# Optimization experiments

Hardware: AMD Instinct MI355X
Metric: run time of the kernel (lower is better)

## Reference

```python
import jax, jax.numpy as jnp
import numpy as np

CONF = 0.3      # confidence threshold (NMS.conf)
IOU = 0.6       # IoU threshold (NMS.iou)
MAX_WH = 4096.0 # class-offset trick for per-class NMS
K = 2048        # max candidates entering NMS (yolov5-style cap)
MAX_DET = 300   # max detections kept per image (fixed output size)


def setup_inputs() -> dict:
    key = jax.random.key(0)
    kxy, kwh, kobj, kcls = jax.random.split(key, 4)
    B, N, NC = 8, 25200, 80
    # realistic raw predictions: xywh in pixel units for a 640x640 image
    xy = jax.random.uniform(kxy, (B, N, 2), minval=0.0, maxval=640.0)
    wh = jax.random.uniform(kwh, (B, N, 2), minval=2.0, maxval=160.0)
    obj = jax.random.uniform(kobj, (B, N, 1))
    cls = jax.random.uniform(kcls, (B, N, NC))
    x = jnp.concatenate([xy, wh, obj, cls], axis=-1)  # [B, N, 5+NC]
    return {"x": x}


def _xywh2xyxy(b):
    xy, half = b[..., :2], b[..., 2:4] * 0.5
    return jnp.concatenate([xy - half, xy + half], axis=-1)


def _pairwise_iou(boxes):  # boxes: [K, 4] xyxy -> [K, K]
    lt = jnp.maximum(boxes[:, None, :2], boxes[None, :, :2])
    rb = jnp.minimum(boxes[:, None, 2:], boxes[None, :, 2:])
    inter = jnp.clip(rb - lt, 0.0).prod(-1)
    area = (boxes[:, 2] - boxes[:, 0]) * (boxes[:, 3] - boxes[:, 1])
    return inter / (area[:, None] + area[None, :] - inter + 1e-9)


def _nms_single(pred):  # pred: [N, 5+NC]
    obj = pred[:, 4]
    cls_conf = pred[:, 5:] * obj[:, None]          # conf = obj * cls prob
    conf = cls_conf.max(-1)
    cls_id = jnp.argmax(cls_conf, -1)
    valid = (obj > CONF) & (conf > CONF)           # candidate + final threshold
    boxes = _xywh2xyxy(pred[:, :4])
    scores = jnp.where(valid, conf, -1.0)
    top_s, idx = jax.lax.top_k(scores, K)          # cap candidates, sorted desc
    boxes_k = boxes[idx]
    cls_k = cls_id[idx]
    valid_k = top_s > 0.0
    # offset boxes by class so NMS is per-class
    shifted = boxes_k + cls_k[:, None].astype(boxes_k.dtype) * MAX_WH
    iou = _pairwise_iou(shifted)                   # [K, K]
    order = jnp.arange(K)

    def body(keep, i):  # greedy suppression in score order
        active = keep[i] & valid_k[i]
        sup = (iou[i] > IOU) & (order > i)
        keep = jnp.where(active, keep & ~sup, keep)
        return keep, None

    keep, _ = jax.lax.scan(body, jnp.ones((K,), bool), order)
    keep = keep & valid_k
    final_s = jnp.where(keep, top_s, -1.0)
    det_s, det_i = jax.lax.top_k(final_s, MAX_DET)
    dets = jnp.concatenate(
        [boxes_k[det_i], top_s[det_i][:, None],
         cls_k[det_i][:, None].astype(boxes_k.dtype)], axis=-1)  # [MAX_DET, 6]
    return dets, det_s > 0.0


def reference(x):
    # returns (dets [B, MAX_DET, 6] = xyxy,conf,cls ; valid mask [B, MAX_DET])
    return jax.vmap(_nms_single)(x)
```

## Files before the change

### kernel.cpp

```cpp
#include <hip/hip_runtime.h>
#include <hip/hip_bf16.h>

#define B 8
#define N 25200
#define ROW 85
#define NC 80
#define K 2048
#define MAXDET 300
#define NBUCKET 16384
#define CAND_CAP 4096
#define NCHUNK 32
#define STILE 64

__global__ void __launch_bounds__(256)
nms_score_kernel(const float* __restrict__ x,
                 float* __restrict__ scores,
                 int* __restrict__ cls_id,
                 unsigned* __restrict__ hist) {
    int b = blockIdx.y;
    int i0 = blockIdx.x * STILE;
    int rows = N - i0; if (rows > STILE) rows = STILE;
    __shared__ float lx[STILE * ROW];
    {
        const float4* s4 = (const float4*)(x + ((size_t)b * N + i0) * ROW);
        float4* d4 = (float4*)lx;
        int nv = rows * ROW / 4;
        for (int k = threadIdx.x; k < nv; k += 256) d4[k] = s4[k];
    }
    __syncthreads();
    int g = threadIdx.x >> 2;
    int q = threadIdx.x & 3;
    if (g >= rows) return;
    const float* p = lx + g * ROW;
    float obj = p[4];
    float best = -1e30f;
    int bc = 127;
    if (obj > 0.3f) {
        #pragma unroll
        for (int k = 0; k < 20; ++k) {
            int c = q + 4 * k;
            float v = __fmul_rn(p[5 + c], obj);
            if (v > best) { best = v; bc = c; }
        }
    }
    #pragma unroll
    for (int m = 1; m < 4; m <<= 1) {
        float ov = __shfl_xor(best, m, 64);
        int   oc = __shfl_xor(bc, m, 64);
        if (ov > best || (ov == best && oc < bc)) { best = ov; bc = oc; }
    }
    if (q == 0) {
        int i = i0 + g;
        float score = (obj > 0.3f && best > 0.3f) ? best : -1.0f;
        scores[b * N + i] = score;
        cls_id[b * N + i] = (bc == 127) ? 0 : bc;
        if (score > 0.0f) {
            int qb = (int)(__fmul_rn(score, 16384.0f));
            if (qb > NBUCKET - 1) qb = NBUCKET - 1;
            atomicAdd(&hist[b * NBUCKET + qb], 1u);
        }
    }
}

__global__ void __launch_bounds__(1024, 1)
nms_select_kernel(const float* __restrict__ scores,
                  const float* __restrict__ x,
                  const int* __restrict__ cls_id,
                  const unsigned* __restrict__ hist,
                  float* __restrict__ top_s,
                  float* __restrict__ boxes,
                  int* __restrict__ clsk,
                  float* __restrict__ shifted,
                  float* __restrict__ area,
                  unsigned long long* __restrict__ keepbits) {
    __shared__ unsigned loff[NBUCKET];
    __shared__ unsigned lcnt16[NBUCKET / 2];
    __shared__ unsigned long long lk[CAND_CAP];
    __shared__ unsigned wsum[16];

    int b = blockIdx.x;
    int t = threadIdx.x;
    int ln = t & 63, wv = t >> 6;
    constexpr int NITER = (N + 1023) / 1024;

    if (t < NCHUNK) keepbits[b * NCHUNK + t] = 0ULL;

    {
        uint4 z = {0u, 0u, 0u, 0u};
        uint4* d2 = (uint4*)lcnt16;
        for (int k = t; k < NBUCKET / 8; k += 1024) d2[k] = z;
    }
    for (int k = t; k < CAND_CAP; k += 1024) lk[k] = 0ULL;

    unsigned v[16];
    int base_j = t * 16;
    unsigned A4 = (unsigned)(NBUCKET - 16 - base_j) / 4;
    {
        const uint4* gh = (const uint4*)(hist + (size_t)b * NBUCKET);
        uint4 u0 = gh[A4 + 0];
        uint4 u1 = gh[A4 + 1];
        uint4 u2 = gh[A4 + 2];
        uint4 u3 = gh[A4 + 3];
        unsigned u[16] = {u0.x,u0.y,u0.z,u0.w, u1.x,u1.y,u1.z,u1.w,
                          u2.x,u2.y,u2.z,u2.w, u3.x,u3.y,u3.z,u3.w};
        #pragma unroll
        for (int k = 0; k < 16; ++k) v[k] = u[15 - k];
    }
    unsigned S = 0;
    #pragma unroll
    for (int k = 0; k < 16; ++k) S += v[k];
    unsigned pref = S;
    #pragma unroll
    for (int o = 1; o < 64; o <<= 1) { unsigned u = __shfl_up(pref, o, 64); if (ln >= o) pref += u; }
    if (ln == 63) wsum[wv] = pref;
    __syncthreads();
    unsigned wbase = 0;
    for (int w = 0; w < wv; ++w) wbase += wsum[w];
    unsigned running = wbase + pref - S;
    {
        unsigned o[16];
        #pragma unroll
        for (int k = 0; k < 16; ++k) { o[15 - k] = running; running += v[k]; }
        ((uint4*)loff)[A4 + 0] = make_uint4(o[0],  o[1],  o[2],  o[3]);
        ((uint4*)loff)[A4 + 1] = make_uint4(o[4],  o[5],  o[6],  o[7]);
        ((uint4*)loff)[A4 + 2] = make_uint4(o[8],  o[9],  o[10], o[11]);
        ((uint4*)loff)[A4 + 3] = make_uint4(o[12], o[13], o[14], o[15]);
    }
    __syncthreads();

    float sreg[NITER];
    #pragma unroll
    for (int r = 0; r < NITER; ++r) {
        int i = t + r * 1024;
        sreg[r] = (i < N) ? scores[b * N + i] : -1.0f;
    }
    #pragma unroll
    for (int r = 0; r < NITER; ++r) {
        float s = sreg[r];
        if (s > 0.0f) {
            int i = t + r * 1024;
            int q = (int)(__fmul_rn(s, 16384.0f));
            if (q > NBUCKET - 1) q = NBUCKET - 1;
            unsigned start = loff[q];
            if (start < CAND_CAP) {
                unsigned sh = (q & 1) * 16;
                unsigned old = atomicAdd(&lcnt16[q >> 1], 1u << sh);
                unsigned rank = (old >> sh) & 0xFFFFu;
                unsigned pos = start + rank;
                if (pos < CAND_CAP) {
                    unsigned long long key =
                        ((unsigned long long)__float_as_uint(s) << 32) | (unsigned)(~i);
                    lk[pos] = key;
                }
            }
        }
    }
    __syncthreads();

    for (int q = t; q < NBUCKET; q += 1024) {
        unsigned start = loff[q];
        if (start < CAND_CAP) {
            unsigned c = (lcnt16[q >> 1] >> ((q & 1) * 16)) & 0xFFFFu;
            unsigned m = c;
            if (m > CAND_CAP - start) m = CAND_CAP - start;
            if (m >= 2) {
                for (unsigned a = start + 1; a < start + m; ++a) {
                    unsigned long long kv = lk[a];
                    unsigned p2 = a;
                    while (p2 > start && lk[p2 - 1] < kv) { lk[p2] = lk[p2 - 1]; --p2; }
                    lk[p2] = kv;
                }
            }
        }
    }
    __syncthreads();

    for (int r = t; r < K; r += 1024) {
        unsigned long long key = lk[r];
        float s;
        int idx;
        float x1, y1, x2, y2;
        int c;
        if (key == 0ULL) {
            s = -1.0f; x1 = y1 = x2 = y2 = 0.0f; c = 0;
        } else {
            s = __uint_as_float((unsigned)(key >> 32));
            idx = (int)(~(unsigned)key);
            const float* p = x + ((size_t)b * N + idx) * ROW;
            float cx = p[0], cy = p[1], w = p[2], h = p[3];
            float hx = __fmul_rn(w, 0.5f);
            float hy = __fmul_rn(h, 0.5f);
            x1 = __fsub_rn(cx, hx); y1 = __fsub_rn(cy, hy);
            x2 = __fadd_rn(cx, hx); y2 = __fadd_rn(cy, hy);
            c = cls_id[b * N + idx];
        }
        int o = b * K + r;
        top_s[o] = s;
        boxes[o * 4 + 0] = x1; boxes[o * 4 + 1] = y1;
        boxes[o * 4 + 2] = x2; boxes[o * 4 + 3] = y2;
        clsk[o] = c;
        float sh = __fmul_rn((float)c, 4096.0f);
        float sx1 = __fadd_rn(x1, sh), sy1 = __fadd_rn(y1, sh);
        float sx2 = __fadd_rn(x2, sh), sy2 = __fadd_rn(y2, sh);
        shifted[o * 4 + 0] = sx1; shifted[o * 4 + 1] = sy1;
        shifted[o * 4 + 2] = sx2; shifted[o * 4 + 3] = sy2;
        area[o] = __fmul_rn(__fsub_rn(sx2, sx1), __fsub_rn(sy2, sy1));
    }
}

__global__ void __launch_bounds__(64)
nms_class_kernel(const float* __restrict__ top_s,
                 const int* __restrict__ clsk,
                 const float* __restrict__ shifted,
                 const float* __restrict__ area,
                 unsigned long long* __restrict__ keepbits) {
    int c = blockIdx.x, b = blockIdx.y;
    int t = threadIdx.x;
    unsigned long long below = (t == 0) ? 0ULL : (~0ULL >> (64 - t));

    __shared__ int srank[K];
    __shared__ unsigned long long skeep[NCHUNK];

    int n = 0;
    for (int ch = 0; ch < NCHUNK; ++ch) {
        int r = ch * 64 + t;
        bool sel = (clsk[b * K + r] == c) && (top_s[b * K + r] > 0.0f);
        unsigned long long m = __ballot(sel);
        if (sel) srank[n + __popcll(m & below)] = r;
        n += __popcll(m);
    }
    __syncthreads();
    if (n == 0) return;

    if (n <= 64) {
        float x1 = 0.f, y1 = 0.f, x2 = 0.f, y2 = 0.f, ar = 0.f;
        int r = -1;
        if (t < n) {
            r = srank[t];
            const float* sb = shifted + ((size_t)b * K + r) * 4;
            x1 = sb[0]; y1 = sb[1]; x2 = sb[2]; y2 = sb[3];
            ar = area[b * K + r];
        }
        unsigned long long keepw = (n == 64) ? ~0ULL : ((1ULL << n) - 1ULL);
        for (int i = 0; i < n; ++i) {
            if (!((keepw >> i) & 1ULL)) continue;
            float bx1 = __shfl(x1, i, 64), by1 = __shfl(y1, i, 64);
            float bx2 = __shfl(x2, i, 64), by2 = __shfl(y2, i, 64);
            float ba  = __shfl(ar, i, 64);
            bool cond = false;
            if (t > i && t < n) {
                float lx = fmaxf(bx1, x1), ly = fmaxf(by1, y1);
                float rx = fminf(bx2, x2), ry = fminf(by2, y2);
                float w = fmaxf(__fsub_rn(rx, lx), 0.0f);
                float h = fmaxf(__fsub_rn(ry, ly), 0.0f);
                float inter = __fmul_rn(w, h);
                float denom = __fadd_rn(__fsub_rn(__fadd_rn(ba, ar), inter), 1e-9f);
                cond = __fdiv_rn(inter, denom) > 0.6f;
            }
            keepw &= ~__ballot(cond);
        }
        if (t < n && ((keepw >> t) & 1ULL))
            atomicOr(&keepbits[b * NCHUNK + (r >> 6)], 1ULL << (r & 63));
        return;
    }

    for (int w = t; w < NCHUNK; w += 64) {
        int lo = w * 64;
        unsigned long long vw;
        if (n >= lo + 64)      vw = ~0ULL;
        else if (n <= lo)      vw = 0ULL;
        else                   vw = (1ULL << (n - lo)) - 1ULL;
        skeep[w] = vw;
    }
    __syncthreads();
    for (int i = 0; i < n; ++i) {
        if (!((skeep[i >> 6] >> (i & 63)) & 1ULL)) continue;
        int ri = srank[i];
        const float* sbi = shifted + ((size_t)b * K + ri) * 4;
        float bx1 = sbi[0], by1 = sbi[1], bx2 = sbi[2], by2 = sbi[3];
        float ba = area[b * K + ri];
        int jb_hi = (n - 1) >> 6;
        for (int jb2 = (i + 1) >> 6; jb2 <= jb_hi; ++jb2) {
            int j = jb2 * 64 + t;
            bool cond = false;
            if (j > i && j < n) {
                int rj = srank[j];
                const float* sbj = shifted + ((size_t)b * K + rj) * 4;
                float x1 = sbj[0], y1 = sbj[1], x2 = sbj[2], y2 = sbj[3];
                float arj = area[b * K + rj];
                float lx = fmaxf(bx1, x1), ly = fmaxf(by1, y1);
                float rx = fminf(bx2, x2), ry = fminf(by2, y2);
                float w = fmaxf(__fsub_rn(rx, lx), 0.0f);
                float h = fmaxf(__fsub_rn(ry, ly), 0.0f);
                float inter = __fmul_rn(w, h);
                float denom = __fadd_rn(__fsub_rn(__fadd_rn(ba, arj), inter), 1e-9f);
                cond = __fdiv_rn(inter, denom) > 0.6f;
            }
            unsigned long long sup = __ballot(cond);
            if (t == 0) skeep[jb2] &= ~sup;
        }
        __syncthreads();
    }
    for (int j = t; j < n; j += 64) {
        if ((skeep[j >> 6] >> (j & 63)) & 1ULL) {
            int r = srank[j];
            atomicOr(&keepbits[b * NCHUNK + (r >> 6)], 1ULL << (r & 63));
        }
    }
}

__global__ void __launch_bounds__(64)
nms_out_kernel(const unsigned long long* __restrict__ keepbits,
               const float* __restrict__ top_s,
               const float* __restrict__ boxes,
               const int* __restrict__ clsk,
               float* __restrict__ out) {
    int b = blockIdx.x;
    int lane = threadIdx.x;
    __shared__ unsigned long long kept[NCHUNK];
    if (lane < NCHUNK) kept[lane] = keepbits[b * NCHUNK + lane];
    __syncthreads();

    int total = 0;
    for (int c = 0; c < NCHUNK; ++c) total += __popcll(kept[c]);

    float* dets  = out + (size_t)b * MAXDET * 6;
    float* flags = out + (size_t)B * MAXDET * 6 + (size_t)b * MAXDET;
    unsigned long long below = (lane == 0) ? 0ULL : (~0ULL >> (64 - lane));
    int kc = 0, nc2 = 0;
    for (int c = 0; c < NCHUNK; ++c) {
        int i = c * 64 + lane;
        unsigned long long m = kept[c];
        bool k = ((m >> lane) & 1ULL) != 0ULL;
        int pc = __popcll(m);
        int slot = k ? (kc + __popcll(m & below))
                     : (total + nc2 + __popcll((~m) & below));
        if (slot < MAXDET) {
            int o = b * K + i;
            dets[slot * 6 + 0] = boxes[o * 4 + 0];
            dets[slot * 6 + 1] = boxes[o * 4 + 1];
            dets[slot * 6 + 2] = boxes[o * 4 + 2];
            dets[slot * 6 + 3] = boxes[o * 4 + 3];
            dets[slot * 6 + 4] = top_s[o];
            dets[slot * 6 + 5] = (float)clsk[o];
            flags[slot] = k ? 1.0f : 0.0f;
        }
        kc += pc;
        nc2 += 64 - pc;
    }
}

extern "C" void kernel_launch(void* const* d_in, const int* in_sizes, int n_in,
                              void* d_out, int out_size, void* d_ws, size_t ws_size,
                              hipStream_t stream) {
    const float* x = (const float*)d_in[0];
    float* out = (float*)d_out;

    char* ws = (char*)d_ws;
    size_t off = 0;
    auto alloc = [&](size_t bytes) -> void* {
        void* p = ws + off;
        off += bytes;
        off = (off + 255) & ~(size_t)255;
        return p;
    };

    float*    scores = (float*)    alloc((size_t)B * N * 4);
    int*      cls_id = (int*)      alloc((size_t)B * N * 4);
    float*    top_s  = (float*)    alloc((size_t)B * K * 4);
    float*    boxes  = (float*)    alloc((size_t)B * K * 4 * 4);
    int*      clsk   = (int*)      alloc((size_t)B * K * 4);
    float*    shifted= (float*)    alloc((size_t)B * K * 4 * 4);
    float*    area   = (float*)    alloc((size_t)B * K * 4);
    unsigned long long* keepbits = (unsigned long long*) alloc((size_t)B * NCHUNK * 8);
    unsigned* hist   = (unsigned*) alloc((size_t)B * NBUCKET * 4);
    (void)ws_size;

    hipMemsetAsync(hist, 0, (size_t)B * NBUCKET * 4, stream);
    nms_score_kernel<<<dim3((N + STILE - 1) / STILE, B), 256, 0, stream>>>(x, scores, cls_id, hist);
    nms_select_kernel<<<B, 1024, 0, stream>>>(scores, x, cls_id, hist,
                                              top_s, boxes, clsk, shifted, area, keepbits);
    nms_class_kernel<<<dim3(NC, B), 64, 0, stream>>>(top_s, clsk, shifted, area, keepbits);
    nms_out_kernel<<<B, 64, 0, stream>>>(keepbits, top_s, boxes, clsk, out);
}
```

Before: 144.5 us.

## Split select kernel into scan, grid-wide placement, and finish kernels

The single per-image select kernel, which ran only 8 blocks, is split into three kernels. A scan kernel writes bucket offsets to global memory. A placement kernel spread over the whole grid scatters candidate keys with global atomics. A finish kernel loads the keys, sorts within buckets and gathers the outputs. This spreads the 25200-element scatter across many CUs instead of 8, at the cost of two extra launches, global atomics and extra workspace memset traffic.

```diff
diff --git a/kernel.cpp b/kernel.cpp
--- a/kernel.cpp
+++ b/kernel.cpp
@@ -62,39 +62,16 @@
     }
 }
 
-__global__ void __launch_bounds__(1024, 1)
-nms_select_kernel(const float* __restrict__ scores,
-                  const float* __restrict__ x,
-                  const int* __restrict__ cls_id,
-                  const unsigned* __restrict__ hist,
-                  float* __restrict__ top_s,
-                  float* __restrict__ boxes,
-                  int* __restrict__ clsk,
-                  float* __restrict__ shifted,
-                  float* __restrict__ area,
-                  unsigned long long* __restrict__ keepbits) {
-    __shared__ unsigned loff[NBUCKET];
-    __shared__ unsigned lcnt16[NBUCKET / 2];
-    __shared__ unsigned long long lk[CAND_CAP];
+__global__ void __launch_bounds__(1024)
+nms_scan_kernel(const unsigned* __restrict__ hist,
+                unsigned* __restrict__ gstart) {
     __shared__ unsigned wsum[16];
-
     int b = blockIdx.x;
     int t = threadIdx.x;
     int ln = t & 63, wv = t >> 6;
-    constexpr int NITER = (N + 1023) / 1024;
-
-    if (t < NCHUNK) keepbits[b * NCHUNK + t] = 0ULL;
-
-    {
-        uint4 z = {0u, 0u, 0u, 0u};
-        uint4* d2 = (uint4*)lcnt16;
-        for (int k = t; k < NBUCKET / 8; k += 1024) d2[k] = z;
-    }
-    for (int k = t; k < CAND_CAP; k += 1024) lk[k] = 0ULL;
 
     unsigned v[16];
-    int base_j = t * 16;
-    unsigned A4 = (unsigned)(NBUCKET - 16 - base_j) / 4;
+    unsigned A4 = (unsigned)(NBUCKET - 16 - t * 16) / 4;
     {
         const uint4* gh = (const uint4*)(hist + (size_t)b * NBUCKET);
         uint4 u0 = gh[A4 + 0];
@@ -121,46 +98,65 @@
         unsigned o[16];
         #pragma unroll
         for (int k = 0; k < 16; ++k) { o[15 - k] = running; running += v[k]; }
-        ((uint4*)loff)[A4 + 0] = make_uint4(o[0],  o[1],  o[2],  o[3]);
-        ((uint4*)loff)[A4 + 1] = make_uint4(o[4],  o[5],  o[6],  o[7]);
-        ((uint4*)loff)[A4 + 2] = make_uint4(o[8],  o[9],  o[10], o[11]);
-        ((uint4*)loff)[A4 + 3] = make_uint4(o[12], o[13], o[14], o[15]);
-    }
-    __syncthreads();
-
-    float sreg[NITER];
-    #pragma unroll
-    for (int r = 0; r < NITER; ++r) {
-        int i = t + r * 1024;
-        sreg[r] = (i < N) ? scores[b * N + i] : -1.0f;
-    }
-    #pragma unroll
-    for (int r = 0; r < NITER; ++r) {
-        float s = sreg[r];
-        if (s > 0.0f) {
-            int i = t + r * 1024;
-            int q = (int)(__fmul_rn(s, 16384.0f));
-            if (q > NBUCKET - 1) q = NBUCKET - 1;
-            unsigned start = loff[q];
-            if (start < CAND_CAP) {
-                unsigned sh = (q & 1) * 16;
-                unsigned old = atomicAdd(&lcnt16[q >> 1], 1u << sh);
-                unsigned rank = (old >> sh) & 0xFFFFu;
-                unsigned pos = start + rank;
-                if (pos < CAND_CAP) {
-                    unsigned long long key =
-                        ((unsigned long long)__float_as_uint(s) << 32) | (unsigned)(~i);
-                    lk[pos] = key;
-                }
+        uint4* gs = (uint4*)(gstart + (size_t)b * NBUCKET);
+        gs[A4 + 0] = make_uint4(o[0],  o[1],  o[2],  o[3]);
+        gs[A4 + 1] = make_uint4(o[4],  o[5],  o[6],  o[7]);
+        gs[A4 + 2] = make_uint4(o[8],  o[9],  o[10], o[11]);
+        gs[A4 + 3] = make_uint4(o[12], o[13], o[14], o[15]);
+    }
+}
+
+__global__ void __launch_bounds__(1024)
+nms_place_kernel(const float* __restrict__ scores,
+                 const unsigned* __restrict__ gstart,
+                 unsigned* __restrict__ gcur,
+                 unsigned long long* __restrict__ gkeys) {
+    int b = blockIdx.y;
+    int i = blockIdx.x * 1024 + threadIdx.x;
+    if (i >= N) return;
+    float s = scores[b * N + i];
+    if (s > 0.0f) {
+        int q = (int)(__fmul_rn(s, 16384.0f));
+        if (q > NBUCKET - 1) q = NBUCKET - 1;
+        unsigned start = gstart[b * NBUCKET + q];
+        if (start < CAND_CAP) {
+            unsigned rank = atomicAdd(&gcur[b * NBUCKET + q], 1u);
+            unsigned pos = start + rank;
+            if (pos < CAND_CAP) {
+                gkeys[(size_t)b * CAND_CAP + pos] =
+                    ((unsigned long long)__float_as_uint(s) << 32) | (unsigned)(~i);
             }
         }
     }
+}
+
+__global__ void __launch_bounds__(1024)
+nms_finish_kernel(const unsigned* __restrict__ gstart,
+                  const unsigned* __restrict__ gcur,
+                  const unsigned long long* __restrict__ gkeys,
+                  const float* __restrict__ x,
+                  const int* __restrict__ cls_id,
+                  float* __restrict__ top_s,
+                  float* __restrict__ boxes,
+                  int* __restrict__ clsk,
+                  float* __restrict__ shifted,
+                  float* __restrict__ area,
+                  unsigned long long* __restrict__ keepbits) {
+    __shared__ unsigned long long lk[CAND_CAP];
+    int b = blockIdx.x;
+    int t = threadIdx.x;
+
+    if (t < NCHUNK) keepbits[b * NCHUNK + t] = 0ULL;
+    {
+        const unsigned long long* gk = gkeys + (size_t)b * CAND_CAP;
+        for (int k = t; k < CAND_CAP; k += 1024) lk[k] = gk[k];
+    }
     __syncthreads();
 
     for (int q = t; q < NBUCKET; q += 1024) {
-        unsigned start = loff[q];
+        unsigned start = gstart[b * NBUCKET + q];
         if (start < CAND_CAP) {
-            unsigned c = (lcnt16[q >> 1] >> ((q & 1) * 16)) & 0xFFFFu;
+            unsigned c = gcur[b * NBUCKET + q];
             unsigned m = c;
             if (m > CAND_CAP - start) m = CAND_CAP - start;
             if (m >= 2) {
@@ -374,11 +370,18 @@
     float*    area   = (float*)    alloc((size_t)B * K * 4);
     unsigned long long* keepbits = (unsigned long long*) alloc((size_t)B * NCHUNK * 8);
     unsigned* hist   = (unsigned*) alloc((size_t)B * NBUCKET * 4);
+    unsigned* gcur   = (unsigned*) alloc((size_t)B * NBUCKET * 4);
+    unsigned long long* gkeys = (unsigned long long*) alloc((size_t)B * CAND_CAP * 8);
+    unsigned* gstart = (unsigned*) alloc((size_t)B * NBUCKET * 4);
     (void)ws_size;
 
-    hipMemsetAsync(hist, 0, (size_t)B * NBUCKET * 4, stream);
+    hipMemsetAsync(hist, 0,
+                   (size_t)B * NBUCKET * 4 + (size_t)B * NBUCKET * 4 + (size_t)B * CAND_CAP * 8,
+                   stream);
     nms_score_kernel<<<dim3((N + STILE - 1) / STILE, B), 256, 0, stream>>>(x, scores, cls_id, hist);
-    nms_select_kernel<<<B, 1024, 0, stream>>>(scores, x, cls_id, hist,
+    nms_scan_kernel<<<B, 1024, 0, stream>>>(hist, gstart);
+    nms_place_kernel<<<dim3((N + 1023) / 1024, B), 1024, 0, stream>>>(scores, gstart, gcur, gkeys);
+    nms_finish_kernel<<<B, 1024, 0, stream>>>(gstart, gcur, gkeys, x, cls_id,
                                               top_s, boxes, clsk, shifted, area, keepbits);
     nms_class_kernel<<<dim3(NC, B), 64, 0, stream>>>(top_s, clsk, shifted, area, keepbits);
     nms_out_kernel<<<B, 64, 0, stream>>>(keepbits, top_s, boxes, clsk, out);
```

Result: slower. 150.3 us (+4.0%).

## Precompute per-class candidate bitmasks, fuse output into class kernel via last-block counter

Applied to the files above, without the earlier changes.

The score kernel now also writes xyxy boxes for every row, so the select kernel gathers one float4 instead of reading scattered raw rows. The select kernel builds per-class bitmasks of candidate ranks in shared memory and writes them out. The class kernel then reads 32 mask words instead of scanning all 2048 clsk/top_s entries per class. The separate output kernel is folded in through an atomic done counter, where the last block per image emits the detections. This removes one launch and redundant scans, at the cost of extra box writes for all rows and threadfence/atomic overhead.

```diff
diff --git a/kernel.cpp b/kernel.cpp
--- a/kernel.cpp
+++ b/kernel.cpp
@@ -16,7 +16,8 @@
 nms_score_kernel(const float* __restrict__ x,
                  float* __restrict__ scores,
                  int* __restrict__ cls_id,
-                 unsigned* __restrict__ hist) {
+                 unsigned* __restrict__ hist,
+                 float4* __restrict__ boxes4) {
     int b = blockIdx.y;
     int i0 = blockIdx.x * STILE;
     int rows = N - i0; if (rows > STILE) rows = STILE;
@@ -54,6 +55,11 @@
         float score = (obj > 0.3f && best > 0.3f) ? best : -1.0f;
         scores[b * N + i] = score;
         cls_id[b * N + i] = (bc == 127) ? 0 : bc;
+        float cx = p[0], cy = p[1], w = p[2], h = p[3];
+        float hx = __fmul_rn(w, 0.5f);
+        float hy = __fmul_rn(h, 0.5f);
+        boxes4[b * N + i] = make_float4(__fsub_rn(cx, hx), __fsub_rn(cy, hy),
+                                        __fadd_rn(cx, hx), __fadd_rn(cy, hy));
         if (score > 0.0f) {
             int qb = (int)(__fmul_rn(score, 16384.0f));
             if (qb > NBUCKET - 1) qb = NBUCKET - 1;
@@ -64,7 +70,7 @@
 
 __global__ void __launch_bounds__(1024, 1)
 nms_select_kernel(const float* __restrict__ scores,
-                  const float* __restrict__ x,
+                  const float4* __restrict__ boxes4,
                   const int* __restrict__ cls_id,
                   const unsigned* __restrict__ hist,
                   float* __restrict__ top_s,
@@ -72,10 +78,12 @@
                   int* __restrict__ clsk,
                   float* __restrict__ shifted,
                   float* __restrict__ area,
-                  unsigned long long* __restrict__ keepbits) {
+                  unsigned long long* __restrict__ keepbits,
+                  unsigned long long* __restrict__ gclsmask) {
     __shared__ unsigned loff[NBUCKET];
     __shared__ unsigned lcnt16[NBUCKET / 2];
     __shared__ unsigned long long lk[CAND_CAP];
+    __shared__ unsigned long long lcm[NC * NCHUNK];
     __shared__ unsigned wsum[16];
 
     int b = blockIdx.x;
@@ -91,10 +99,10 @@
         for (int k = t; k < NBUCKET / 8; k += 1024) d2[k] = z;
     }
     for (int k = t; k < CAND_CAP; k += 1024) lk[k] = 0ULL;
+    for (int k = t; k < NC * NCHUNK; k += 1024) lcm[k] = 0ULL;
 
     unsigned v[16];
-    int base_j = t * 16;
-    unsigned A4 = (unsigned)(NBUCKET - 16 - base_j) / 4;
+    unsigned A4 = (unsigned)(NBUCKET - 16 - t * 16) / 4;
     {
         const uint4* gh = (const uint4*)(hist + (size_t)b * NBUCKET);
         uint4 u0 = gh[A4 + 0];
@@ -186,13 +194,10 @@
         } else {
             s = __uint_as_float((unsigned)(key >> 32));
             idx = (int)(~(unsigned)key);
-            const float* p = x + ((size_t)b * N + idx) * ROW;
-            float cx = p[0], cy = p[1], w = p[2], h = p[3];
-            float hx = __fmul_rn(w, 0.5f);
-            float hy = __fmul_rn(h, 0.5f);
-            x1 = __fsub_rn(cx, hx); y1 = __fsub_rn(cy, hy);
-            x2 = __fadd_rn(cx, hx); y2 = __fadd_rn(cy, hy);
+            float4 bb = boxes4[(size_t)b * N + idx];
+            x1 = bb.x; y1 = bb.y; x2 = bb.z; y2 = bb.w;
             c = cls_id[b * N + idx];
+            atomicOr(&lcm[c * NCHUNK + (r >> 6)], 1ULL << (r & 63));
         }
         int o = b * K + r;
         top_s[o] = s;
@@ -206,14 +211,21 @@
         shifted[o * 4 + 2] = sx2; shifted[o * 4 + 3] = sy2;
         area[o] = __fmul_rn(__fsub_rn(sx2, sx1), __fsub_rn(sy2, sy1));
     }
+    __syncthreads();
+    for (int k = t; k < NC * NCHUNK; k += 1024)
+        gclsmask[(size_t)b * NC * NCHUNK + k] = lcm[k];
 }
 
 __global__ void __launch_bounds__(64)
-nms_class_kernel(const float* __restrict__ top_s,
-                 const int* __restrict__ clsk,
-                 const float* __restrict__ shifted,
-                 const float* __restrict__ area,
-                 unsigned long long* __restrict__ keepbits) {
+nms_classout_kernel(const unsigned long long* __restrict__ gclsmask,
+                    const float* __restrict__ top_s,
+                    const int* __restrict__ clsk,
+                    const float* __restrict__ shifted,
+                    const float* __restrict__ area,
+                    const float* __restrict__ boxes,
+                    unsigned long long* __restrict__ keepbits,
+                    unsigned* __restrict__ done_ctr,
+                    float* __restrict__ out) {
     int c = blockIdx.x, b = blockIdx.y;
     int t = threadIdx.x;
     unsigned long long below = (t == 0) ? 0ULL : (~0ULL >> (64 - t));
@@ -221,18 +233,17 @@
     __shared__ int srank[K];
     __shared__ unsigned long long skeep[NCHUNK];
 
+    const unsigned long long* cm = gclsmask + ((size_t)b * NC + c) * NCHUNK;
     int n = 0;
+    #pragma unroll 4
     for (int ch = 0; ch < NCHUNK; ++ch) {
-        int r = ch * 64 + t;
-        bool sel = (clsk[b * K + r] == c) && (top_s[b * K + r] > 0.0f);
-        unsigned long long m = __ballot(sel);
-        if (sel) srank[n + __popcll(m & below)] = r;
+        unsigned long long m = cm[ch];
+        if ((m >> t) & 1ULL) srank[n + __popcll(m & below)] = ch * 64 + t;
         n += __popcll(m);
     }
     __syncthreads();
-    if (n == 0) return;
-
-    if (n <= 64) {
+
+    if (n > 0 && n <= 64) {
         float x1 = 0.f, y1 = 0.f, x2 = 0.f, y2 = 0.f, ar = 0.f;
         int r = -1;
         if (t < n) {
@@ -261,92 +272,89 @@
         }
         if (t < n && ((keepw >> t) & 1ULL))
             atomicOr(&keepbits[b * NCHUNK + (r >> 6)], 1ULL << (r & 63));
-        return;
-    }
-
-    for (int w = t; w < NCHUNK; w += 64) {
-        int lo = w * 64;
-        unsigned long long vw;
-        if (n >= lo + 64)      vw = ~0ULL;
-        else if (n <= lo)      vw = 0ULL;
-        else                   vw = (1ULL << (n - lo)) - 1ULL;
-        skeep[w] = vw;
-    }
-    __syncthreads();
-    for (int i = 0; i < n; ++i) {
-        if (!((skeep[i >> 6] >> (i & 63)) & 1ULL)) continue;
-        int ri = srank[i];
-        const float* sbi = shifted + ((size_t)b * K + ri) * 4;
-        float bx1 = sbi[0], by1 = sbi[1], bx2 = sbi[2], by2 = sbi[3];
-        float ba = area[b * K + ri];
-        int jb_hi = (n - 1) >> 6;
-        for (int jb2 = (i + 1) >> 6; jb2 <= jb_hi; ++jb2) {
-            int j = jb2 * 64 + t;
-            bool cond = false;
-            if (j > i && j < n) {
-                int rj = srank[j];
-                const float* sbj = shifted + ((size_t)b * K + rj) * 4;
-                float x1 = sbj[0], y1 = sbj[1], x2 = sbj[2], y2 = sbj[3];
-                float arj = area[b * K + rj];
-                float lx = fmaxf(bx1, x1), ly = fmaxf(by1, y1);
-                float rx = fminf(bx2, x2), ry = fminf(by2, y2);
-                float w = fmaxf(__fsub_rn(rx, lx), 0.0f);
-                float h = fmaxf(__fsub_rn(ry, ly), 0.0f);
-                float inter = __fmul_rn(w, h);
-                float denom = __fadd_rn(__fsub_rn(__fadd_rn(ba, arj), inter), 1e-9f);
-                cond = __fdiv_rn(inter, denom) > 0.6f;
-            }
-            unsigned long long sup = __ballot(cond);
-            if (t == 0) skeep[jb2] &= ~sup;
+    } else if (n > 64) {
+        for (int w = t; w < NCHUNK; w += 64) {
+            int lo = w * 64;
+            unsigned long long vw;
+            if (n >= lo + 64)      vw = ~0ULL;
+            else if (n <= lo)      vw = 0ULL;
+            else                   vw = (1ULL << (n - lo)) - 1ULL;
+            skeep[w] = vw;
         }
         __syncthreads();
-    }
-    for (int j = t; j < n; j += 64) {
-        if ((skeep[j >> 6] >> (j & 63)) & 1ULL) {
-            int r = srank[j];
-            atomicOr(&keepbits[b * NCHUNK + (r >> 6)], 1ULL << (r & 63));
-        }
-    }
-}
-
-__global__ void __launch_bounds__(64)
-nms_out_kernel(const unsigned long long* __restrict__ keepbits,
-               const float* __restrict__ top_s,
-               const float* __restrict__ boxes,
-               const int* __restrict__ clsk,
-               float* __restrict__ out) {
-    int b = blockIdx.x;
-    int lane = threadIdx.x;
-    __shared__ unsigned long long kept[NCHUNK];
-    if (lane < NCHUNK) kept[lane] = keepbits[b * NCHUNK + lane];
-    __syncthreads();
-
-    int total = 0;
-    for (int c = 0; c < NCHUNK; ++c) total += __popcll(kept[c]);
-
-    float* dets  = out + (size_t)b * MAXDET * 6;
-    float* flags = out + (size_t)B * MAXDET * 6 + (size_t)b * MAXDET;
-    unsigned long long below = (lane == 0) ? 0ULL : (~0ULL >> (64 - lane));
-    int kc = 0, nc2 = 0;
-    for (int c = 0; c < NCHUNK; ++c) {
-        int i = c * 64 + lane;
-        unsigned long long m = kept[c];
-        bool k = ((m >> lane) & 1ULL) != 0ULL;
-        int pc = __popcll(m);
-        int slot = k ? (kc + __popcll(m & below))
-                     : (total + nc2 + __popcll((~m) & below));
-        if (slot < MAXDET) {
-            int o = b * K + i;
-            dets[slot * 6 + 0] = boxes[o * 4 + 0];
-            dets[slot * 6 + 1] = boxes[o * 4 + 1];
-            dets[slot * 6 + 2] = boxes[o * 4 + 2];
-            dets[slot * 6 + 3] = boxes[o * 4 + 3];
-            dets[slot * 6 + 4] = top_s[o];
-            dets[slot * 6 + 5] = (float)clsk[o];
-            flags[slot] = k ? 1.0f : 0.0f;
-        }
-        kc += pc;
-        nc2 += 64 - pc;
+        for (int i = 0; i < n; ++i) {
+            if (!((skeep[i >> 6] >> (i & 63)) & 1ULL)) continue;
+            int ri = srank[i];
+            const float* sbi = shifted + ((size_t)b * K + ri) * 4;
+            float bx1 = sbi[0], by1 = sbi[1], bx2 = sbi[2], by2 = sbi[3];
+            float ba = area[b * K + ri];
+            int jb_hi = (n - 1) >> 6;
+            for (int jb2 = (i + 1) >> 6; jb2 <= jb_hi; ++jb2) {
+                int j = jb2 * 64 + t;
+                bool cond = false;
+                if (j > i && j < n) {
+                    int rj = srank[j];
+                    const float* sbj = shifted + ((size_t)b * K + rj) * 4;
+                    float x1 = sbj[0], y1 = sbj[1], x2 = sbj[2], y2 = sbj[3];
+                    float arj = area[b * K + rj];
+                    float lx = fmaxf(bx1, x1), ly = fmaxf(by1, y1);
+                    float rx = fminf(bx2, x2), ry = fminf(by2, y2);
+                    float w = fmaxf(__fsub_rn(rx, lx), 0.0f);
+                    float h = fmaxf(__fsub_rn(ry, ly), 0.0f);
+                    float inter = __fmul_rn(w, h);
+                    float denom = __fadd_rn(__fsub_rn(__fadd_rn(ba, arj), inter), 1e-9f);
+                    cond = __fdiv_rn(inter, denom) > 0.6f;
+                }
+                unsigned long long sup = __ballot(cond);
+                if (t == 0) skeep[jb2] &= ~sup;
+            }
+            __syncthreads();
+        }
+        for (int j = t; j < n; j += 64) {
+            if ((skeep[j >> 6] >> (j & 63)) & 1ULL) {
+                int r = srank[j];
+                atomicOr(&keepbits[b * NCHUNK + (r >> 6)], 1ULL << (r & 63));
+            }
+        }
+    }
+
+    __threadfence();
+    unsigned old = 0;
+    if (t == 0) old = atomicAdd(&done_ctr[b], 1u);
+    old = (unsigned)__shfl((int)old, 0, 64);
+    if (old == NC - 1) {
+        __threadfence();
+        __shared__ unsigned long long kept[NCHUNK];
+        if (t < NCHUNK)
+            kept[t] = atomicOr(&keepbits[b * NCHUNK + t], 0ULL);
+        __syncthreads();
+
+        int total = 0;
+        for (int ch = 0; ch < NCHUNK; ++ch) total += __popcll(kept[ch]);
+
+        float* dets  = out + (size_t)b * MAXDET * 6;
+        float* flags = out + (size_t)B * MAXDET * 6 + (size_t)b * MAXDET;
+        int kc = 0, nc2 = 0;
+        for (int ch = 0; ch < NCHUNK; ++ch) {
+            int i = ch * 64 + t;
+            unsigned long long m = kept[ch];
+            bool k = ((m >> t) & 1ULL) != 0ULL;
+            int pc = __popcll(m);
+            int slot = k ? (kc + __popcll(m & below))
+                         : (total + nc2 + __popcll((~m) & below));
+            if (slot < MAXDET) {
+                int o = b * K + i;
+                dets[slot * 6 + 0] = boxes[o * 4 + 0];
+                dets[slot * 6 + 1] = boxes[o * 4 + 1];
+                dets[slot * 6 + 2] = boxes[o * 4 + 2];
+                dets[slot * 6 + 3] = boxes[o * 4 + 3];
+                dets[slot * 6 + 4] = top_s[o];
+                dets[slot * 6 + 5] = (float)clsk[o];
+                flags[slot] = k ? 1.0f : 0.0f;
+            }
+            kc += pc;
+            nc2 += 64 - pc;
+        }
     }
 }
 
@@ -367,19 +375,25 @@
 
     float*    scores = (float*)    alloc((size_t)B * N * 4);
     int*      cls_id = (int*)      alloc((size_t)B * N * 4);
+    float4*   boxes4 = (float4*)   alloc((size_t)B * N * 16);
     float*    top_s  = (float*)    alloc((size_t)B * K * 4);
     float*    boxes  = (float*)    alloc((size_t)B * K * 4 * 4);
     int*      clsk   = (int*)      alloc((size_t)B * K * 4);
     float*    shifted= (float*)    alloc((size_t)B * K * 4 * 4);
     float*    area   = (float*)    alloc((size_t)B * K * 4);
     unsigned long long* keepbits = (unsigned long long*) alloc((size_t)B * NCHUNK * 8);
-    unsigned* hist   = (unsigned*) alloc((size_t)B * NBUCKET * 4);
+    unsigned long long* gclsmask = (unsigned long long*) alloc((size_t)B * NC * NCHUNK * 8);
+    unsigned* hist     = (unsigned*) alloc((size_t)B * NBUCKET * 4);
+    unsigned* done_ctr = (unsigned*) alloc(256);
     (void)ws_size;
 
-    hipMemsetAsync(hist, 0, (size_t)B * NBUCKET * 4, stream);
-    nms_score_kernel<<<dim3((N + STILE - 1) / STILE, B), 256, 0, stream>>>(x, scores, cls_id, hist);
-    nms_select_kernel<<<B, 1024, 0, stream>>>(scores, x, cls_id, hist,
-                                              top_s, boxes, clsk, shifted, area, keepbits);
-    nms_class_kernel<<<dim3(NC, B), 64, 0, stream>>>(top_s, clsk, shifted, area, keepbits);
-    nms_out_kernel<<<B, 64, 0, stream>>>(keepbits, top_s, boxes, clsk, out);
+    hipMemsetAsync(hist, 0, (size_t)B * NBUCKET * 4 + 256, stream);
+    nms_score_kernel<<<dim3((N + STILE - 1) / STILE, B), 256, 0, stream>>>(
+        x, scores, cls_id, hist, boxes4);
+    nms_select_kernel<<<B, 1024, 0, stream>>>(scores, boxes4, cls_id, hist,
+                                              top_s, boxes, clsk, shifted, area,
+                                              keepbits, gclsmask);
+    nms_classout_kernel<<<dim3(NC, B), 64, 0, stream>>>(gclsmask, top_s, clsk,
+                                                        shifted, area, boxes,
+                                                        keepbits, done_ctr, out);
 }
```

Result: no change. 142.7 us (-1.2%).
